# Optimization experiments

Hardware: AMD Instinct MI355X
Metric: run time of the kernel (lower is better)

## Reference

```python
import jax, jax.numpy as jnp
from jax import lax
import numpy as np

SEQ, BATCH, IN, HID = 1024, 8192, 3, 50


def setup_inputs() -> dict:
    key = jax.random.key(0)
    ks = jax.random.split(key, 7)
    s_ih = 1.0 / np.sqrt(HID)
    return {
        "x": jax.random.normal(ks[0], (SEQ, BATCH, IN), dtype=jnp.float32),
        "W_ih": jax.random.normal(ks[1], (4 * HID, IN), dtype=jnp.float32) * s_ih,
        "W_hh": jax.random.normal(ks[2], (4 * HID, HID), dtype=jnp.float32) * s_ih,
        "b_ih": jax.random.normal(ks[3], (4 * HID,), dtype=jnp.float32) * s_ih,
        "b_hh": jax.random.normal(ks[4], (4 * HID,), dtype=jnp.float32) * s_ih,
        "fc_w": jax.random.normal(ks[5], (1, HID), dtype=jnp.float32) * s_ih,
        "fc_b": jax.random.normal(ks[6], (1,), dtype=jnp.float32) * s_ih,
    }


def reference(x, W_ih, W_hh, b_ih, b_hh, fc_w, fc_b):
    # x: (T, B, I); PyTorch LSTM gate order is i, f, g, o along the 4H axis.
    T, B, _ = x.shape
    H = W_hh.shape[1]
    # Hoist the input projection out of the recurrence: one big GEMM.
    xg = jnp.einsum("tbi,gi->tbg", x, W_ih) + b_ih + b_hh  # (T, B, 4H)

    def step(carry, xg_t):
        h, c = carry
        gates = xg_t + h @ W_hh.T  # (B, 4H)
        i, f, g, o = jnp.split(gates, 4, axis=-1)
        i = jax.nn.sigmoid(i)
        f = jax.nn.sigmoid(f)
        g = jnp.tanh(g)
        o = jax.nn.sigmoid(o)
        c = f * c + i * g
        h = o * jnp.tanh(c)
        return (h, c), None

    h0 = jnp.zeros((B, H), dtype=x.dtype)
    c0 = jnp.zeros((B, H), dtype=x.dtype)
    (h_last, _), _ = lax.scan(step, (h0, c0), xg)
    # h.squeeze(0) in the torch code -> last layer's final hidden state (B, H)
    return h_last @ fc_w.T + fc_b  # (B, 1)
```

## Files before the change

kernel.cpp:

```cpp
#include <hip/hip_runtime.h>

#define SEQ   1024
#define BATCH 8192
#define HID   50
#define BT    16
#define CHS   16
#define NCH   (SEQ/CHS)
#define CHF   (CHS*BT*3)

typedef _Float16 half8 __attribute__((ext_vector_type(8)));
typedef float    f32x4 __attribute__((ext_vector_type(4)));

__device__ __forceinline__ int bslot(int k, int b){
  return (k >> 5)*512 + ((k & 31) >> 3)*128 + b*8 + (k & 7);
}

#define XLD(cg) {                                                          \
    const int s0_ = (tid*683) >> 15;                                       \
    xr0 = x[(size_t)(((cg)*CHS + s0_)*BATCH + b0)*3 + (tid - 48*s0_)];     \
    if (tid < 256) {                                                       \
      const int f1 = tid + 512; const int s1_ = (f1*683) >> 15;            \
      xr1 = x[(size_t)(((cg)*CHS + s1_)*BATCH + b0)*3 + (f1 - 48*s1_)];    \
    } }

#define ELEM(acc, C, slot) {                                                           \
    const float si = __builtin_amdgcn_rcpf(1.0f + __builtin_amdgcn_exp2f((acc)[0]));   \
    const float sf = __builtin_amdgcn_rcpf(1.0f + __builtin_amdgcn_exp2f((acc)[1]));   \
    const float rg = __builtin_amdgcn_rcpf(1.0f + __builtin_amdgcn_exp2f((acc)[2]));   \
    const float so = __builtin_amdgcn_rcpf(1.0f + __builtin_amdgcn_exp2f((acc)[3]));   \
    const float G  = __builtin_fmaf(-5.77078016355584f, rg, 2.88539008177792f);        \
    C = __builtin_fmaf(sf, C, si*G);                                                   \
    const float r2 = __builtin_amdgcn_rcpf(1.0f + __builtin_amdgcn_exp2f(C));          \
    const float u_ = so * r2;                                                          \
    const float h_ = __builtin_fmaf(-2.0f, u_, so);                                    \
    Bst[q][slot] = (_Float16)h_; }

__global__ __launch_bounds__(512, 4)
void lstm_w8(const float* __restrict__ x,
             const float* __restrict__ W_ih,
             const float* __restrict__ W_hh,
             const float* __restrict__ b_ih,
             const float* __restrict__ b_hh,
             const float* __restrict__ fc_w,
             const float* __restrict__ fc_b,
             float* __restrict__ out)
{
  __shared__ _Float16 Bst[2][1024];
  __shared__ float    xb[2][CHF];

  const int tid  = threadIdx.x;
  const int w    = tid >> 6;
  const int lane = tid & 63;
  const int r16  = lane & 15;
  const int grp  = lane >> 4;
  const int b0   = blockIdx.x * BT;
  const float L2E = 1.44269504088896f;

  half8 Af[2][2];
  #pragma unroll
  for (int it = 0; it < 2; ++it) {
    const int tile = it ? (8 + w) : w;
    #pragma unroll
    for (int kh = 0; kh < 2; ++kh) {
      half8 f;
      #pragma unroll
      for (int i = 0; i < 8; ++i) {
        const int k = kh*32 + grp*8 + i;
        const int c = tile*16 + r16;
        float wv = 0.0f;
        if (tile < 13 && c < 4*HID) {
          const int j = c >> 2, gi = c & 3;
          const int go = gi*HID + j;
          const float sc = (gi == 2) ? (2.0f*L2E) : (-L2E);
          if (k < HID)      wv = W_hh[go*HID + k] * sc;
          else if (k < 53)  wv = W_ih[go*3 + (k-50)] * sc;
          else if (k == 53) wv = (b_ih[go] + b_hh[go]) * sc;
        }
        f[i] = (_Float16)wv;
      }
      Af[it][kh] = f;
    }
  }

  const int j1t = 32 + w*4 + grp;
  const int ws0 = bslot(w*4 + grp, r16);
  const int ws1 = bslot((j1t < HID) ? j1t : 0, r16);

  for (int i = tid; i < 1024; i += 512) ((unsigned*)Bst)[i] = 0u;
  __syncthreads();
  if (tid < 32) Bst[tid >> 4][768 + (tid & 15)*8 + 5] = (_Float16)1.0f;

  float xr0 = 0.f, xr1 = 0.f;
  XLD(0); xb[0][tid] = xr0; if (tid < 256) xb[0][tid+512] = xr1;
  XLD(1); xb[1][tid] = xr0; if (tid < 256) xb[1][tid+512] = xr1;
  XLD(2);
  __syncthreads();
  if (tid < 48) {
    const int bb = (tid*171) >> 9, e = tid - 3*bb;
    Bst[0][768 + bb*8 + 2 + e] = (_Float16)xb[0][tid];
  }
  __syncthreads();

  float cs0 = 0.f, cs1 = 0.f;

  auto step = [&](int t, int p, int q) {
    const half8 s0 = *(const half8*)&Bst[p][lane*8];
    const half8 s1 = *(const half8*)&Bst[p][512 + lane*8];
    f32x4 a0 = {0.f,0.f,0.f,0.f};
    a0 = __builtin_amdgcn_mfma_f32_16x16x32_f16(Af[0][0], s0, a0, 0,0,0);
    a0 = __builtin_amdgcn_mfma_f32_16x16x32_f16(Af[0][1], s1, a0, 0,0,0);
    if (w < 5) {
      f32x4 a1 = {0.f,0.f,0.f,0.f};
      a1 = __builtin_amdgcn_mfma_f32_16x16x32_f16(Af[1][0], s0, a1, 0,0,0);
      a1 = __builtin_amdgcn_mfma_f32_16x16x32_f16(Af[1][1], s1, a1, 0,0,0);
      ELEM(a0, cs0, ws0);
      if (w < 4 || grp < 2) ELEM(a1, cs1, ws1);
    } else {
      ELEM(a0, cs0, ws0);
    }
    if (w == 6 && lane < 48) {
      const int tn = t + 1;
      const int bb = (lane*171) >> 9, e = lane - 3*bb;
      Bst[q][768 + bb*8 + 2 + e] = (_Float16)xb[(tn >> 4) & 1][(tn & 15)*48 + lane];
    }
    asm volatile("s_waitcnt lgkmcnt(0)\n\ts_barrier" ::: "memory");
  };

  #pragma unroll 1
  for (int tc = 0; tc < NCH; ++tc) {
    if (tc > 0) {
      const int pc = (tc + 1) & 1;
      xb[pc][tid] = xr0;
      if (tid < 256) xb[pc][tid + 512] = xr1;
      if (tc + 2 < NCH) { XLD(tc+2); }
    }
    const int tb = tc*CHS;
    #pragma unroll 1
    for (int u = 0; u < CHS/2; ++u) {
      step(tb + 2*u,     0, 1);
      step(tb + 2*u + 1, 1, 0);
    }
  }

  if (tid < BT) {
    float s = fc_b[0];
    #pragma unroll
    for (int j = 0; j < HID; ++j)
      s += fc_w[j] * (float)Bst[0][bslot(j, tid)];
    out[b0 + tid] = s;
  }
}

extern "C" void kernel_launch(void* const* d_in, const int* in_sizes, int n_in,
                              void* d_out, int out_size, void* d_ws, size_t ws_size,
                              hipStream_t stream)
{
  const float* x    = (const float*)d_in[0];
  const float* W_ih = (const float*)d_in[1];
  const float* W_hh = (const float*)d_in[2];
  const float* b_ih = (const float*)d_in[3];
  const float* b_hh = (const float*)d_in[4];
  const float* fc_w = (const float*)d_in[5];
  const float* fc_b = (const float*)d_in[6];
  lstm_w8<<<BATCH/BT, 512, 0, stream>>>(x, W_ih, W_hh, b_ih, b_hh, fc_w, fc_b,
                                        (float*)d_out);
}
```

Before: 589.4 us.

## Process two 16-column batch groups per block with rebalanced gate tiles

Each block now handles 32 batch columns as two independent 16-column groups that share the same weight fragments in registers, halving the grid to 256 blocks. The second weight tile assignment is rebalanced so that waves 0-1 and 5-7 do extra work for group B while waves 0-4 do it for group A, spreading MFMA and elementwise work more evenly. Each step barrier now covers two groups, so barrier and LDS-latency cost per batch column drops. In exchange each step does more serial work per wave and fewer blocks run, with occupancy hinted at 2 blocks per CU and 64KB of dynamic shared memory requested.

```diff
diff --git a/kernel.cpp b/kernel.cpp
--- a/kernel.cpp
+++ b/kernel.cpp
@@ -3,7 +3,7 @@
 #define SEQ   1024
 #define BATCH 8192
 #define HID   50
-#define BT    16
+#define BT    32
 #define CHS   16
 #define NCH   (SEQ/CHS)
 #define CHF   (CHS*BT*3)
@@ -15,15 +15,17 @@
   return (k >> 5)*512 + ((k & 31) >> 3)*128 + b*8 + (k & 7);
 }
 
+#define MFMA16(A,B,C) __builtin_amdgcn_mfma_f32_16x16x32_f16(A,B,C,0,0,0)
+
 #define XLD(cg) {                                                          \
-    const int s0_ = (tid*683) >> 15;                                       \
-    xr0 = x[(size_t)(((cg)*CHS + s0_)*BATCH + b0)*3 + (tid - 48*s0_)];     \
-    if (tid < 256) {                                                       \
-      const int f1 = tid + 512; const int s1_ = (f1*683) >> 15;            \
-      xr1 = x[(size_t)(((cg)*CHS + s1_)*BATCH + b0)*3 + (f1 - 48*s1_)];    \
-    } }
+    const int f1 = tid + 512, f2 = tid + 1024;                             \
+    const int s0_ = (tid*683) >> 16, s1_ = (f1*683) >> 16,                 \
+              s2_ = (f2*683) >> 16;                                        \
+    xr0 = x[(size_t)(((cg)*CHS + s0_)*BATCH + b0)*3 + (tid - 96*s0_)];     \
+    xr1 = x[(size_t)(((cg)*CHS + s1_)*BATCH + b0)*3 + (f1  - 96*s1_)];     \
+    xr2 = x[(size_t)(((cg)*CHS + s2_)*BATCH + b0)*3 + (f2  - 96*s2_)]; }
 
-#define ELEM(acc, C, slot) {                                                           \
+#define ELEM(acc, C, bq, slot) {                                                       \
     const float si = __builtin_amdgcn_rcpf(1.0f + __builtin_amdgcn_exp2f((acc)[0]));   \
     const float sf = __builtin_amdgcn_rcpf(1.0f + __builtin_amdgcn_exp2f((acc)[1]));   \
     const float rg = __builtin_amdgcn_rcpf(1.0f + __builtin_amdgcn_exp2f((acc)[2]));   \
@@ -32,11 +34,10 @@
     C = __builtin_fmaf(sf, C, si*G);                                                   \
     const float r2 = __builtin_amdgcn_rcpf(1.0f + __builtin_amdgcn_exp2f(C));          \
     const float u_ = so * r2;                                                          \
-    const float h_ = __builtin_fmaf(-2.0f, u_, so);                                    \
-    Bst[q][slot] = (_Float16)h_; }
+    (bq)[slot] = (_Float16)__builtin_fmaf(-2.0f, u_, so); }
 
-__global__ __launch_bounds__(512, 4)
-void lstm_w8(const float* __restrict__ x,
+__global__ __launch_bounds__(512, 2)
+void lstm_g2(const float* __restrict__ x,
              const float* __restrict__ W_ih,
              const float* __restrict__ W_hh,
              const float* __restrict__ b_ih,
@@ -45,7 +46,7 @@
              const float* __restrict__ fc_b,
              float* __restrict__ out)
 {
-  __shared__ _Float16 Bst[2][1024];
+  __shared__ _Float16 Bst[2][2][1024];
   __shared__ float    xb[2][CHF];
 
   const int tid  = threadIdx.x;
@@ -56,10 +57,15 @@
   const int b0   = blockIdx.x * BT;
   const float L2E = 1.44269504088896f;
 
+  const int  t1    = w;
+  const int  t2    = (w < 5) ? (8 + w) : (5 + w);
+  const bool hasA2 = (w < 5);
+  const bool hasB2 = (w < 2) || (w >= 5);
+
   half8 Af[2][2];
   #pragma unroll
   for (int it = 0; it < 2; ++it) {
-    const int tile = it ? (8 + w) : w;
+    const int tile = it ? t2 : t1;
     #pragma unroll
     for (int kh = 0; kh < 2; ++kh) {
       half8 f;
@@ -68,7 +74,7 @@
         const int k = kh*32 + grp*8 + i;
         const int c = tile*16 + r16;
         float wv = 0.0f;
-        if (tile < 13 && c < 4*HID) {
+        if (c < 4*HID) {
           const int j = c >> 2, gi = c & 3;
           const int go = gi*HID + j;
           const float sc = (gi == 2) ? (2.0f*L2E) : (-L2E);
@@ -82,46 +88,57 @@
     }
   }
 
-  const int j1t = 32 + w*4 + grp;
-  const int ws0 = bslot(w*4 + grp, r16);
-  const int ws1 = bslot((j1t < HID) ? j1t : 0, r16);
+  const int j2  = t2*4 + grp;
+  const int ws1 = bslot(t1*4 + grp, r16);
+  const int ws2 = bslot((j2 < HID) ? j2 : 0, r16);
+  const bool m2 = (j2 < HID);
 
-  for (int i = tid; i < 1024; i += 512) ((unsigned*)Bst)[i] = 0u;
+  #pragma unroll
+  for (int i = 0; i < 4; ++i) ((unsigned*)Bst)[tid + 512*i] = 0u;
   __syncthreads();
-  if (tid < 32) Bst[tid >> 4][768 + (tid & 15)*8 + 5] = (_Float16)1.0f;
+  if (tid < 64) Bst[tid >> 5][(tid >> 4) & 1][768 + (tid & 15)*8 + 5] = (_Float16)1.0f;
 
-  float xr0 = 0.f, xr1 = 0.f;
-  XLD(0); xb[0][tid] = xr0; if (tid < 256) xb[0][tid+512] = xr1;
-  XLD(1); xb[1][tid] = xr0; if (tid < 256) xb[1][tid+512] = xr1;
+  float xr0, xr1, xr2;
+  XLD(0); xb[0][tid] = xr0; xb[0][tid+512] = xr1; xb[0][tid+1024] = xr2;
+  XLD(1); xb[1][tid] = xr0; xb[1][tid+512] = xr1; xb[1][tid+1024] = xr2;
   XLD(2);
   __syncthreads();
-  if (tid < 48) {
-    const int bb = (tid*171) >> 9, e = tid - 3*bb;
-    Bst[0][768 + bb*8 + 2 + e] = (_Float16)xb[0][tid];
+  if (tid < 96) {
+    const int g = tid >= 48, l = tid - 48*g;
+    const int bb = (l*171) >> 9, e = l - 3*bb;
+    Bst[g][0][768 + bb*8 + 2 + e] = (_Float16)xb[0][tid];
   }
   __syncthreads();
 
-  float cs0 = 0.f, cs1 = 0.f;
+  float csA0 = 0.f, csA1 = 0.f, csB0 = 0.f, csB1 = 0.f;
 
   auto step = [&](int t, int p, int q) {
-    const half8 s0 = *(const half8*)&Bst[p][lane*8];
-    const half8 s1 = *(const half8*)&Bst[p][512 + lane*8];
-    f32x4 a0 = {0.f,0.f,0.f,0.f};
-    a0 = __builtin_amdgcn_mfma_f32_16x16x32_f16(Af[0][0], s0, a0, 0,0,0);
-    a0 = __builtin_amdgcn_mfma_f32_16x16x32_f16(Af[0][1], s1, a0, 0,0,0);
-    if (w < 5) {
-      f32x4 a1 = {0.f,0.f,0.f,0.f};
-      a1 = __builtin_amdgcn_mfma_f32_16x16x32_f16(Af[1][0], s0, a1, 0,0,0);
-      a1 = __builtin_amdgcn_mfma_f32_16x16x32_f16(Af[1][1], s1, a1, 0,0,0);
-      ELEM(a0, cs0, ws0);
-      if (w < 4 || grp < 2) ELEM(a1, cs1, ws1);
-    } else {
-      ELEM(a0, cs0, ws0);
+    _Float16* bqA = &Bst[0][q][0];
+    _Float16* bqB = &Bst[1][q][0];
+    const half8 sA0 = *(const half8*)&Bst[0][p][lane*8];
+    const half8 sA1 = *(const half8*)&Bst[0][p][512 + lane*8];
+    const half8 sB0 = *(const half8*)&Bst[1][p][lane*8];
+    const half8 sB1 = *(const half8*)&Bst[1][p][512 + lane*8];
+    f32x4 aA0 = {0.f,0.f,0.f,0.f}, aB0 = {0.f,0.f,0.f,0.f};
+    aA0 = MFMA16(Af[0][0], sA0, aA0);  aA0 = MFMA16(Af[0][1], sA1, aA0);
+    aB0 = MFMA16(Af[0][0], sB0, aB0);  aB0 = MFMA16(Af[0][1], sB1, aB0);
+    if (hasA2) {
+      f32x4 aA1 = {0.f,0.f,0.f,0.f};
+      aA1 = MFMA16(Af[1][0], sA0, aA1);  aA1 = MFMA16(Af[1][1], sA1, aA1);
+      if (m2) ELEM(aA1, csA1, bqA, ws2);
     }
-    if (w == 6 && lane < 48) {
+    if (hasB2) {
+      f32x4 aB1 = {0.f,0.f,0.f,0.f};
+      aB1 = MFMA16(Af[1][0], sB0, aB1);  aB1 = MFMA16(Af[1][1], sB1, aB1);
+      if (m2) ELEM(aB1, csB1, bqB, ws2);
+    }
+    ELEM(aA0, csA0, bqA, ws1);
+    ELEM(aB0, csB0, bqB, ws1);
+    if ((w == 2 || w == 3) && lane < 48) {
       const int tn = t + 1;
       const int bb = (lane*171) >> 9, e = lane - 3*bb;
-      Bst[q][768 + bb*8 + 2 + e] = (_Float16)xb[(tn >> 4) & 1][(tn & 15)*48 + lane];
+      const float xv = xb[(tn >> 4) & 1][(tn & 15)*96 + (w - 2)*48 + lane];
+      (w == 2 ? bqA : bqB)[768 + bb*8 + 2 + e] = (_Float16)xv;
     }
     asm volatile("s_waitcnt lgkmcnt(0)\n\ts_barrier" ::: "memory");
   };
@@ -130,8 +147,7 @@
   for (int tc = 0; tc < NCH; ++tc) {
     if (tc > 0) {
       const int pc = (tc + 1) & 1;
-      xb[pc][tid] = xr0;
-      if (tid < 256) xb[pc][tid + 512] = xr1;
+      xb[pc][tid] = xr0; xb[pc][tid+512] = xr1; xb[pc][tid+1024] = xr2;
       if (tc + 2 < NCH) { XLD(tc+2); }
     }
     const int tb = tc*CHS;
@@ -142,11 +158,13 @@
     }
   }
 
+  __syncthreads();
   if (tid < BT) {
+    const int g = tid >> 4, b = tid & 15;
     float s = fc_b[0];
     #pragma unroll
     for (int j = 0; j < HID; ++j)
-      s += fc_w[j] * (float)Bst[0][bslot(j, tid)];
+      s += fc_w[j] * (float)Bst[g][0][bslot(j, b)];
     out[b0 + tid] = s;
   }
 }
@@ -162,6 +180,6 @@
   const float* b_hh = (const float*)d_in[4];
   const float* fc_w = (const float*)d_in[5];
   const float* fc_b = (const float*)d_in[6];
-  lstm_w8<<<BATCH/BT, 512, 0, stream>>>(x, W_ih, W_hh, b_ih, b_hh, fc_w, fc_b,
-                                        (float*)d_out);
+  lstm_g2<<<BATCH/BT, 512, 65536, stream>>>(x, W_ih, W_hh, b_ih, b_hh, fc_w, fc_b,
+                                            (float*)d_out);
 }
```

Result: faster. 542.0 us (median of 2 runs) (-8.0%).
